# Optimization experiments

Hardware: AMD Instinct MI355X
Metric: run time of the kernel (lower is better)

## Reference

```python
import jax, jax.numpy as jnp
import numpy as np

B, L, H, D, VOC, C, P = 16, 256, 6, 768, 32000, 20, 1
d = D // H
MAXF = 20
BN_EPS = 1e-5


def setup_inputs() -> dict:
    key = jax.random.key(0)
    ks = jax.random.split(key, 8)
    doc_tids = jax.random.randint(ks[0], (B, L), 0, VOC)
    TFs = jax.random.uniform(ks[1], (B, L), dtype=jnp.float32) * 20.0 + 1.0
    DFs = jax.random.uniform(ks[2], (B, L), dtype=jnp.float32) * 1000.0 + 1.0
    emb = jax.random.normal(ks[3], (VOC, D), dtype=jnp.float32) * 0.02
    fcW = jax.random.normal(ks[4], (C + P, D), dtype=jnp.float32) * 0.02
    fcb = jnp.zeros((C + P,), dtype=jnp.float32)
    weiW = jax.random.normal(ks[5], (2, H), dtype=jnp.float32) * 0.1
    weib = jnp.zeros((2,), dtype=jnp.float32)
    return dict(doc_tids=doc_tids, TFs=TFs, DFs=DFs, emb=emb,
                fcW=fcW, fcb=fcb, weiW=weiW, weib=weib)


def _bn(x):
    # BatchNorm over channel axis 1 (H), batch stats over all other axes (train mode, affine=False)
    m = x.mean(axis=(0, 2, 3), keepdims=True)
    v = x.var(axis=(0, 2, 3), keepdims=True)
    return (x - m) * jax.lax.rsqrt(v + BN_EPS)


def _leaky9(x):
    return jnp.where(x >= 0, x, 9.0 * x)


def reference(doc_tids, TFs, DFs, emb, fcW, fcb, weiW, weib):
    # --- EmbbedingTFIDF (eval mode, dropout off): tf-idf weighted embedding lookup ---
    tf = jnp.minimum(TFs, float(MAXF))
    idf = jnp.log1p(1.0 / DFs)
    x = emb[doc_tids] * (tf * idf)[:, :, None]          # (B, L, D)
    valid = doc_tids != 0
    # model flips pad_mask with logical_not, then co_weights[pad_mask] = 0
    invalid = ~(valid[:, :, None] & valid[:, None, :])  # (B, L, L) True -> zero out
    mask = invalid[:, None, :, :]                       # broadcast over heads

    def split_heads(h):
        return h.reshape(B, L, H, d).transpose(0, 2, 1, 3)  # (B, H, L, d)

    Q = split_heads(x)
    K = Q
    V = Q

    # --- nearAttention (layers=1) ---
    Vn = _bn(V)
    # DistMatrix: pairwise Euclidean distance dist[b,h,i,j] = ||K_i - Q_j||
    Ksq = jnp.sum(K * K, axis=-1)[..., :, None]
    Qsq = jnp.sum(Q * Q, axis=-1)[..., None, :]
    cross = jnp.einsum('bhid,bhjd->bhij', K, Q)
    co = jnp.sqrt(jnp.maximum(Ksq + Qsq - 2.0 * cross, 1e-12))  # (B, H, L, L)
    # BatchNorm1d(H) over flattened (B, H, L*L) == per-H stats over (0,2,3)
    co = _leaky9(_bn(co))
    co = jnp.where(mask, 0.0, co)
    co = jax.nn.softmax(co, axis=-1)
    co = jnp.where(jnp.isnan(co), 0.0, co)
    V_out = jnp.einsum('bhij,bhjd->bhid', co, Vn)
    Q_out = _bn(jnp.einsum('bhij,bhjd->bhid', co, Q))
    K_out = _bn(jnp.einsum('bhij,bhjd->bhid', co, K))

    # --- head ---
    Vc = V_out.transpose(0, 2, 1, 3).reshape(B, L, D)       # catHiddens
    V_lgts = jax.nn.softmax(Vc @ fcW.T + fcb, axis=-1)      # (B, L, C+P)
    cw = jnp.swapaxes(co, -1, -2).reshape(B, L * L, H)      # transpose then contiguous reshape
    cw = jax.nn.softmax(cw @ weiW.T + weib, axis=-1)        # (B, L*L, 2)
    cw = cw.reshape(B, L, L, 2).sum(axis=-2, keepdims=True)[:, :, :, 0]  # (B, L, 1)
    cw = jax.nn.softmax(cw, axis=-1)                        # softmax over singleton -> ones (faithful)
    logits = (cw * V_lgts).sum(axis=1)[:, :C]               # (B, C)
    logits = jax.nn.softmax(logits, axis=-1)
    return logits
```

## Files before the change

### kernel.cpp

```cpp
#include <hip/hip_runtime.h>
#include <hip/hip_bf16.h>
#include <math.h>

#define OFF_XH   0UL
#define OFF_XT   1572864UL
#define OFF_VC   3145728UL
#define OFF_SQ   4718592UL
#define OFF_THS  4743168UL
#define OFF_PART 4767744UL
#define OFF_STAT 4780032UL
#define OFF_ACC  4780056UL
#define OFF_CTR  4780392UL
#define OFF_FCWB 4780396UL

typedef __attribute__((ext_vector_type(8))) __bf16 bf16x8;
typedef __attribute__((ext_vector_type(4))) float f32x4;
typedef __attribute__((ext_vector_type(8))) unsigned short u16x8;

__global__ __launch_bounds__(512) void k12_fused(const int* __restrict__ tids,
    const float* __restrict__ TF, const float* __restrict__ DF,
    const float* __restrict__ emb, unsigned short* __restrict__ xh,
    unsigned short* __restrict__ xT, float* __restrict__ sq,
    float* __restrict__ part, const float* __restrict__ fcW,
    unsigned short* __restrict__ fcWb, float* __restrict__ acc,
    unsigned int* __restrict__ ctr) {
  int jh = blockIdx.x, bh = blockIdx.y;
  int b = bh / 6, h = bh % 6;
  int tid = threadIdx.x;
  __shared__ unsigned short tile[32768];
  __shared__ float swd1[8], swd2[8], swv1[8], swv2[8];
  if (jh == 1) {
    if (tid < 168) {
      int idx = bh * 168 + tid;
      fcWb[idx] = __bfloat16_as_ushort(__float2bfloat16(fcW[idx]));
    }
  } else if (bh == 0) {
    if (tid < 336) acc[tid] = 0.0f;
    if (tid == 336) *ctr = 0u;
  }
  int sub = tid & 7, row0 = tid >> 3;
  int c16 = sub * 16;
  float ts1 = 0.0f, ts2 = 0.0f;
#pragma unroll
  for (int p = 0; p < 4; ++p) {
    int r = p * 64 + row0;
    int tok = b * 256 + r;
    int tv = tids[tok];
    float wgt = fminf(TF[tok], 20.0f) * log1pf(1.0f / DF[tok]);
    const float* er = emb + (size_t)tv * 768 + h * 128 + c16;
    float4 e0 = *(const float4*)er;
    float4 e1 = *(const float4*)(er + 4);
    float4 e2 = *(const float4*)(er + 8);
    float4 e3 = *(const float4*)(er + 12);
    float f[16] = {e0.x, e0.y, e0.z, e0.w, e1.x, e1.y, e1.z, e1.w,
                   e2.x, e2.y, e2.z, e2.w, e3.x, e3.y, e3.z, e3.w};
    u16x8 pk0, pk1;
    float s1 = 0.0f, s2 = 0.0f;
#pragma unroll
    for (int e = 0; e < 8; ++e) {
      __hip_bfloat16 hb = __float2bfloat16(f[e] * wgt);
      float g = __bfloat162float(hb);
      s1 += g; s2 += g * g;
      pk0[e] = __bfloat16_as_ushort(hb);
    }
#pragma unroll
    for (int e = 0; e < 8; ++e) {
      __hip_bfloat16 hb = __float2bfloat16(f[8 + e] * wgt);
      float g = __bfloat162float(hb);
      s1 += g; s2 += g * g;
      pk1[e] = __bfloat16_as_ushort(hb);
    }
    ts1 += s1; ts2 += s2;
    int rx = r & 7;
    *(u16x8*)&tile[r * 128 + (((sub * 2    ) ^ rx) * 8)] = pk0;
    *(u16x8*)&tile[r * 128 + (((sub * 2 + 1) ^ rx) * 8)] = pk1;
    if (jh == 0) {
      unsigned short* xo = xh + ((size_t)bh * 256 + r) * 128 + c16;
      *(u16x8*)xo = pk0;
      *(u16x8*)(xo + 8) = pk1;
    }
    s2 += __shfl_down(s2, 4); s2 += __shfl_down(s2, 2); s2 += __shfl_down(s2, 1);
    if (sub == 0)
      sq[(size_t)bh * 256 + r] = s2;
  }
  __syncthreads();
  if (jh == 1) {
    int ch = tid & 127, q = tid >> 7;
    int cc = ch >> 3, cs = ch & 7;
    unsigned int* xo = (unsigned int*)xT + ((size_t)bh * 128 + ch) * 128 + q * 32;
#pragma unroll
    for (int g = 0; g < 8; ++g) {
      unsigned int tmp[4];
#pragma unroll
      for (int k = 0; k < 4; ++k) {
        int t0 = q * 64 + (g * 4 + k) * 2;
        unsigned int lo = tile[ t0      * 128 + ((cc ^ ( t0      & 7)) * 8) + cs];
        unsigned int hi = tile[(t0 + 1) * 128 + ((cc ^ ((t0 + 1) & 7)) * 8) + cs];
        tmp[k] = lo | (hi << 16);
      }
      uint4 vv; vv.x = tmp[0]; vv.y = tmp[1]; vv.z = tmp[2]; vv.w = tmp[3];
      *(uint4*)(xo + g * 4) = vv;
    }
  }
  int w = tid >> 6, lane = tid & 63, quad = lane >> 4, l16 = lane & 15;
  const float* sqh = sq + (size_t)bh * 256;
  int it0 = w * 2;
  bf16x8 a2[2][4];
  float si2[2][4];
#pragma unroll
  for (int ith = 0; ith < 2; ++ith) {
    int ar = (it0 + ith) * 16 + l16, arx = ar & 7;
#pragma unroll
    for (int k0 = 0; k0 < 4; ++k0)
      a2[ith][k0] = *(const bf16x8*)&tile[ar * 128 + (((k0 * 4 + quad) ^ arx) * 8)];
#pragma unroll
    for (int r = 0; r < 4; ++r)
      si2[ith][r] = sqh[(it0 + ith) * 16 + quad * 4 + r];
  }
  float ls1 = 0.0f, ls2 = 0.0f;
#pragma unroll
  for (int jt = 0; jt < 8; ++jt) {
    int jr = jh * 128 + jt * 16 + l16, jrx = jr & 7;
    bf16x8 bfr[4];
#pragma unroll
    for (int k0 = 0; k0 < 4; ++k0)
      bfr[k0] = *(const bf16x8*)&tile[jr * 128 + (((k0 * 4 + quad) ^ jrx) * 8)];
    f32x4 acc0 = {0.0f, 0.0f, 0.0f, 0.0f}, acc1 = {0.0f, 0.0f, 0.0f, 0.0f};
#pragma unroll
    for (int k0 = 0; k0 < 4; ++k0) {
      acc0 = __builtin_amdgcn_mfma_f32_16x16x32_bf16(a2[0][k0], bfr[k0], acc0, 0, 0, 0);
      acc1 = __builtin_amdgcn_mfma_f32_16x16x32_bf16(a2[1][k0], bfr[k0], acc1, 0, 0, 0);
    }
    float sj = sqh[jr];
#pragma unroll
    for (int r = 0; r < 4; ++r) {
      float cv0 = sqrtf(fmaxf(si2[0][r] + sj - 2.0f * acc0[r], 1e-12f));
      float cv1 = sqrtf(fmaxf(si2[1][r] + sj - 2.0f * acc1[r], 1e-12f));
      ls1 += cv0 + cv1;
      ls2 += cv0 * cv0 + cv1 * cv1;
    }
  }
#pragma unroll
  for (int off = 32; off >= 1; off >>= 1) {
    ls1 += __shfl_down(ls1, off);
    ls2 += __shfl_down(ls2, off);
    ts1 += __shfl_down(ts1, off);
    ts2 += __shfl_down(ts2, off);
  }
  if (lane == 0) { swd1[w] = ls1; swd2[w] = ls2; swv1[w] = ts1; swv2[w] = ts2; }
  __syncthreads();
  if (tid == 0) {
    float d1 = 0.0f, d2 = 0.0f, v1 = 0.0f, v2 = 0.0f;
#pragma unroll
    for (int i = 0; i < 8; ++i) { d1 += swd1[i]; d2 += swd2[i]; v1 += swv1[i]; v2 += swv2[i]; }
    part[192 + (bh * 2 + jh) * 2 + 0] = d1;
    part[192 + (bh * 2 + jh) * 2 + 1] = d2;
    if (jh == 0) { part[bh * 2] = v1; part[bh * 2 + 1] = v2; }
  }
}

__global__ __launch_bounds__(256, 4) void k45_fused(const unsigned short* __restrict__ xh,
    const unsigned short* __restrict__ xT, const int* __restrict__ tids,
    const float* __restrict__ sq, const float* __restrict__ part,
    unsigned short* __restrict__ vc16) {
  int bid = blockIdx.x;
  int xcd = bid & 7, idx = bid >> 3;
  int bh = xcd * 12 + idx % 12;
  int p = idx / 12;
  int b = bh / 6, h = bh % 6;
  int tid = threadIdx.x, w = tid >> 6, lane = tid & 63;
  int quad = lane >> 4, l16 = lane & 15;
  int I = p * 16;
  __shared__ float svld[256];
  __shared__ float ssq[256];
  __shared__ unsigned short cot[16][264];
  __shared__ float smax[16][4];
  __shared__ float ssum[16][4];
  __shared__ float sstat[4];
  svld[tid] = (tids[b * 256 + tid] != 0) ? 1.0f : 0.0f;
  ssq[tid] = sq[(size_t)bh * 256 + tid];
  if (w == 0) {
    float c1 = 0.0f, c2 = 0.0f;
    if (lane < 32) {
      int bb = lane >> 1, jj = lane & 1;
      c1 = part[192 + ((bb * 6 + h) * 2 + jj) * 2 + 0];
      c2 = part[192 + ((bb * 6 + h) * 2 + jj) * 2 + 1];
    }
#pragma unroll
    for (int off = 16; off >= 1; off >>= 1) {
      c1 += __shfl_down(c1, off);
      c2 += __shfl_down(c2, off);
    }
    float v1 = 0.0f, v2 = 0.0f;
    if (lane < 16) {
      v1 = part[(lane * 6 + h) * 2 + 0];
      v2 = part[(lane * 6 + h) * 2 + 1];
    }
#pragma unroll
    for (int off = 8; off >= 1; off >>= 1) {
      v1 += __shfl_down(v1, off);
      v2 += __shfl_down(v2, off);
    }
    if (lane == 0) {
      float mean = c1 / 1048576.0f;
      float var = c2 / 1048576.0f - mean * mean;
      sstat[0] = mean;
      sstat[1] = rsqrtf(var + 1e-5f);
      float mv = v1 / 524288.0f;
      float vv = v2 / 524288.0f - mv * mv;
      sstat[2] = mv;
      sstat[3] = rsqrtf(vv + 1e-5f);
    }
  }
  const __bf16* xb = (const __bf16*)xh + (size_t)bh * 256 * 128;
  bf16x8 a[4];
#pragma unroll
  for (int k0 = 0; k0 < 4; ++k0)
    a[k0] = *(const bf16x8*)(xb + (size_t)(I + l16) * 128 + k0 * 32 + quad * 8);
  __syncthreads();
  float m = sstat[0], rsc = sstat[1];
  float rv[4], si[4];
#pragma unroll
  for (int r = 0; r < 4; ++r) {
    rv[r] = svld[I + quad * 4 + r];
    si[r] = ssq[I + quad * 4 + r];
  }
  float y[4][4];
#pragma unroll
  for (int tl = 0; tl < 4; ++tl) {
    int t = w * 4 + tl;
    f32x4 acc = {0.0f, 0.0f, 0.0f, 0.0f};
#pragma unroll
    for (int k0 = 0; k0 < 4; ++k0) {
      bf16x8 bfr = *(const bf16x8*)(xb + (size_t)(t * 16 + l16) * 128 + k0 * 32 + quad * 8);
      acc = __builtin_amdgcn_mfma_f32_16x16x32_bf16(a[k0], bfr, acc, 0, 0, 0);
    }
    float sj = ssq[t * 16 + l16];
    float cvld = svld[t * 16 + l16];
#pragma unroll
    for (int r = 0; r < 4; ++r) {
      float cv = sqrtf(fmaxf(si[r] + sj - 2.0f * acc[r], 1e-12f));
      float yv = (cv - m) * rsc;
      yv = yv >= 0.0f ? yv : 9.0f * yv;
      y[tl][r] = yv * rv[r] * cvld;
    }
  }
#pragma unroll
  for (int r = 0; r < 4; ++r) {
    float mx = fmaxf(fmaxf(y[0][r], y[1][r]), fmaxf(y[2][r], y[3][r]));
#pragma unroll
    for (int off = 1; off <= 8; off <<= 1) mx = fmaxf(mx, __shfl_xor(mx, off));
    if (l16 == 0) smax[quad * 4 + r][w] = mx;
  }
  __syncthreads();
  float gmx[4];
#pragma unroll
  for (int r = 0; r < 4; ++r) {
    int row = quad * 4 + r;
    gmx[r] = fmaxf(fmaxf(smax[row][0], smax[row][1]), fmaxf(smax[row][2], smax[row][3]));
    float s = 0.0f;
#pragma unroll
    for (int tl = 0; tl < 4; ++tl) { y[tl][r] = expf(y[tl][r] - gmx[r]); s += y[tl][r]; }
#pragma unroll
    for (int off = 1; off <= 8; off <<= 1) s += __shfl_xor(s, off);
    if (l16 == 0) ssum[row][w] = s;
  }
  __syncthreads();
#pragma unroll
  for (int r = 0; r < 4; ++r) {
    int row = quad * 4 + r;
    float gs = ssum[row][0] + ssum[row][1] + ssum[row][2] + ssum[row][3];
    float inv = 1.0f / gs;
#pragma unroll
    for (int tl = 0; tl < 4; ++tl)
      cot[row][w * 64 + tl * 16 + l16] =
          __bfloat16_as_ushort(__float2bfloat16(y[tl][r] * inv));
  }
  __syncthreads();
  bf16x8 a2[8];
#pragma unroll
  for (int k0 = 0; k0 < 8; ++k0)
    a2[k0] = *(const bf16x8*)&cot[l16][k0 * 32 + quad * 8];
  const __bf16* xbT = (const __bf16*)xT + (size_t)bh * 128 * 256;
  float mv = sstat[2], rvs = sstat[3];
  float rm = rvs * mv;
  size_t vbase = ((size_t)(b * 256 + I + quad * 4)) * 768 + h * 128;
#pragma unroll
  for (int jl = 0; jl < 2; ++jl) {
    int ch = (w * 2 + jl) * 16 + l16;
    const __bf16* brow = xbT + (size_t)ch * 256;
    f32x4 vacc = {0.0f, 0.0f, 0.0f, 0.0f};
#pragma unroll
    for (int k0 = 0; k0 < 8; ++k0) {
      bf16x8 bfr = *(const bf16x8*)(brow + k0 * 32 + quad * 8);
      vacc = __builtin_amdgcn_mfma_f32_16x16x32_bf16(a2[k0], bfr, vacc, 0, 0, 0);
    }
#pragma unroll
    for (int r = 0; r < 4; ++r) {
      float ov = rvs * vacc[r] - rm;
      vc16[vbase + (size_t)r * 768 + ch] = __bfloat16_as_ushort(__float2bfloat16(ov));
    }
  }
}

__global__ __launch_bounds__(256) void k5b6_lgts(const unsigned short* __restrict__ vc16,
    const unsigned short* __restrict__ fcWb, const float* __restrict__ fcb,
    float* __restrict__ acc, unsigned int* __restrict__ ctr, float* __restrict__ out) {
  int b = blockIdx.x >> 2, qa = blockIdx.x & 3;
  int tid = threadIdx.x, w = tid >> 6, lane = tid & 63;
  int quad = lane >> 4, l16 = lane & 15;
  int tok0 = b * 256 + qa * 64 + w * 16;
  int c1c = (l16 < 5) ? (16 + l16) : 20;
  const __bf16* vb = (const __bf16*)vc16;
  const __bf16* w0 = (const __bf16*)fcWb + (size_t)l16 * 768;
  const __bf16* w1 = (const __bf16*)fcWb + (size_t)c1c * 768;
  f32x4 ac0 = {0.0f, 0.0f, 0.0f, 0.0f}, ac1 = {0.0f, 0.0f, 0.0f, 0.0f};
#pragma unroll
  for (int k0 = 0; k0 < 24; ++k0) {
    int ko = k0 * 32 + quad * 8;
    bf16x8 af = *(const bf16x8*)(vb + (size_t)(tok0 + l16) * 768 + ko);
    bf16x8 b0 = *(const bf16x8*)(w0 + ko);
    bf16x8 b1 = *(const bf16x8*)(w1 + ko);
    ac0 = __builtin_amdgcn_mfma_f32_16x16x32_bf16(af, b0, ac0, 0, 0, 0);
    ac1 = __builtin_amdgcn_mfma_f32_16x16x32_bf16(af, b1, ac1, 0, 0, 0);
  }
  float bias0 = fcb[l16];
  float bias1 = (l16 < 5) ? fcb[16 + l16] : 0.0f;
  float p0s = 0.0f, p1s = 0.0f;
#pragma unroll
  for (int r = 0; r < 4; ++r) {
    float lg0 = ac0[r] + bias0;
    float lg1 = (l16 < 5) ? (ac1[r] + bias1) : -1e30f;
    float mx = fmaxf(lg0, lg1);
#pragma unroll
    for (int off = 1; off <= 8; off <<= 1) mx = fmaxf(mx, __shfl_xor(mx, off));
    float e0 = expf(lg0 - mx), e1 = expf(lg1 - mx);
    float s = e0 + e1;
#pragma unroll
    for (int off = 1; off <= 8; off <<= 1) s += __shfl_xor(s, off);
    float inv = 1.0f / s;
    p0s += e0 * inv;
    p1s += e1 * inv;
  }
  p0s += __shfl_xor(p0s, 16); p0s += __shfl_xor(p0s, 32);
  p1s += __shfl_xor(p1s, 16); p1s += __shfl_xor(p1s, 32);
  __shared__ float sacc[4][21];
  __shared__ unsigned int sdone;
  if (quad == 0) sacc[w][l16] = p0s;
  if (quad == 1 && l16 < 5) sacc[w][16 + l16] = p1s;
  __syncthreads();
  if (tid < 21) {
    float s = sacc[0][tid] + sacc[1][tid] + sacc[2][tid] + sacc[3][tid];
    atomicAdd(&acc[b * 21 + tid], s);
  }
  __syncthreads();
  if (tid == 0) {
    __threadfence();
    sdone = atomicAdd(ctr, 1u);
  }
  __syncthreads();
  if (sdone == 63u && tid < 16) {
    float v[20];
    float mx = -1e30f;
#pragma unroll
    for (int c = 0; c < 20; ++c) {
      v[c] = atomicAdd(&acc[tid * 21 + c], 0.0f);
      mx = fmaxf(mx, v[c]);
    }
    float s = 0.0f;
#pragma unroll
    for (int c = 0; c < 20; ++c) { v[c] = expf(v[c] - mx); s += v[c]; }
    float inv = 1.0f / s;
#pragma unroll
    for (int c = 0; c < 20; ++c) out[tid * 20 + c] = v[c] * inv;
  }
}

extern "C" void kernel_launch(void* const* d_in, const int* in_sizes, int n_in,
                              void* d_out, int out_size, void* d_ws, size_t ws_size,
                              hipStream_t stream) {
  const int*   tids = (const int*)d_in[0];
  const float* TF   = (const float*)d_in[1];
  const float* DF   = (const float*)d_in[2];
  const float* emb  = (const float*)d_in[3];
  const float* fcW  = (const float*)d_in[4];
  const float* fcb  = (const float*)d_in[5];
  float* out = (float*)d_out;
  float* ws  = (float*)d_ws;
  unsigned short* xh   = (unsigned short*)(ws + OFF_XH);
  unsigned short* xT   = (unsigned short*)(ws + OFF_XT);
  unsigned short* vc   = (unsigned short*)(ws + OFF_VC);
  unsigned short* fcWb = (unsigned short*)(ws + OFF_FCWB);
  float* sq    = ws + OFF_SQ;
  float* part  = ws + OFF_PART;
  float* acc   = ws + OFF_ACC;
  unsigned int* ctr = (unsigned int*)(ws + OFF_CTR);

  k12_fused<<<dim3(2, 96), 512, 0, stream>>>(tids, TF, DF, emb, xh, xT, sq, part,
                                             fcW, fcWb, acc, ctr);
  k45_fused<<<1536, 256, 0, stream>>>(xh, xT, tids, sq, part, vc);
  k5b6_lgts<<<64, 256, 0, stream>>>(vc, fcWb, fcb, acc, ctr, out);
}
```

Baseline: 193.6 us.

## Fuse attention and logits kernels into one per-row-tile kernel over all heads

The attention kernel and the classifier-logits kernel are merged. Each 512-thread block now handles one batch and a 16-row tile across all six heads sequentially, keeping the concatenated V output in shared memory instead of writing it to global memory. The fc projection, per-token softmax and batch accumulation then run from shared memory. This removes a kernel launch and the global round trip of the V buffer. In exchange the grid shrinks from 1536 to 256 blocks, and the loop over heads is serialised with extra barriers, which may reduce parallelism and latency hiding.

```diff
diff --git a/kernel.cpp b/kernel.cpp
--- a/kernel.cpp
+++ b/kernel.cpp
@@ -4,11 +4,8 @@
 
 #define OFF_XH   0UL
 #define OFF_XT   1572864UL
-#define OFF_VC   3145728UL
 #define OFF_SQ   4718592UL
-#define OFF_THS  4743168UL
 #define OFF_PART 4767744UL
-#define OFF_STAT 4780032UL
 #define OFF_ACC  4780056UL
 #define OFF_CTR  4780392UL
 #define OFF_FCWB 4780396UL
@@ -159,27 +156,34 @@
   }
 }
 
-__global__ __launch_bounds__(256, 4) void k45_fused(const unsigned short* __restrict__ xh,
+__global__ __launch_bounds__(512) void k456_fused(const unsigned short* __restrict__ xh,
     const unsigned short* __restrict__ xT, const int* __restrict__ tids,
     const float* __restrict__ sq, const float* __restrict__ part,
-    unsigned short* __restrict__ vc16) {
+    const unsigned short* __restrict__ fcWb, const float* __restrict__ fcb,
+    float* __restrict__ acc, unsigned int* __restrict__ ctr, float* __restrict__ out) {
   int bid = blockIdx.x;
   int xcd = bid & 7, idx = bid >> 3;
-  int bh = xcd * 12 + idx % 12;
-  int p = idx / 12;
-  int b = bh / 6, h = bh % 6;
+  int b = xcd * 2 + (idx >> 4);
+  int p = idx & 15;
   int tid = threadIdx.x, w = tid >> 6, lane = tid & 63;
   int quad = lane >> 4, l16 = lane & 15;
   int I = p * 16;
   __shared__ float svld[256];
-  __shared__ float ssq[256];
+  __shared__ float ssqall[1536];
   __shared__ unsigned short cot[16][264];
-  __shared__ float smax[16][4];
-  __shared__ float ssum[16][4];
-  __shared__ float sstat[4];
-  svld[tid] = (tids[b * 256 + tid] != 0) ? 1.0f : 0.0f;
-  ssq[tid] = sq[(size_t)bh * 256 + tid];
-  if (w == 0) {
+  __shared__ float smax[16][8];
+  __shared__ float ssum[16][8];
+  __shared__ float sstat[24];
+  __shared__ unsigned short vct[16][776];
+  __shared__ float sacc[16][22];
+  __shared__ float facc[21];
+  __shared__ unsigned int sdone;
+  if (tid < 256) svld[tid] = (tids[b * 256 + tid] != 0) ? 1.0f : 0.0f;
+  for (int i = tid; i < 1536; i += 512) ssqall[i] = sq[(size_t)b * 1536 + i];
+  if (tid < 352) ((float*)sacc)[tid] = 0.0f;
+  if (tid >= 352 && tid < 373) facc[tid - 352] = 0.0f;
+  if (w < 6) {
+    int h = w;
     float c1 = 0.0f, c2 = 0.0f;
     if (lane < 32) {
       int bb = lane >> 1, jj = lane & 1;
@@ -204,90 +208,92 @@
     if (lane == 0) {
       float mean = c1 / 1048576.0f;
       float var = c2 / 1048576.0f - mean * mean;
-      sstat[0] = mean;
-      sstat[1] = rsqrtf(var + 1e-5f);
+      sstat[h * 4 + 0] = mean;
+      sstat[h * 4 + 1] = rsqrtf(var + 1e-5f);
       float mv = v1 / 524288.0f;
       float vv = v2 / 524288.0f - mv * mv;
-      sstat[2] = mv;
-      sstat[3] = rsqrtf(vv + 1e-5f);
-    }
-  }
-  const __bf16* xb = (const __bf16*)xh + (size_t)bh * 256 * 128;
-  bf16x8 a[4];
-#pragma unroll
-  for (int k0 = 0; k0 < 4; ++k0)
-    a[k0] = *(const bf16x8*)(xb + (size_t)(I + l16) * 128 + k0 * 32 + quad * 8);
-  __syncthreads();
-  float m = sstat[0], rsc = sstat[1];
-  float rv[4], si[4];
-#pragma unroll
-  for (int r = 0; r < 4; ++r) {
-    rv[r] = svld[I + quad * 4 + r];
-    si[r] = ssq[I + quad * 4 + r];
-  }
-  float y[4][4];
-#pragma unroll
-  for (int tl = 0; tl < 4; ++tl) {
-    int t = w * 4 + tl;
-    f32x4 acc = {0.0f, 0.0f, 0.0f, 0.0f};
-#pragma unroll
-    for (int k0 = 0; k0 < 4; ++k0) {
-      bf16x8 bfr = *(const bf16x8*)(xb + (size_t)(t * 16 + l16) * 128 + k0 * 32 + quad * 8);
-      acc = __builtin_amdgcn_mfma_f32_16x16x32_bf16(a[k0], bfr, acc, 0, 0, 0);
-    }
-    float sj = ssq[t * 16 + l16];
-    float cvld = svld[t * 16 + l16];
-#pragma unroll
-    for (int r = 0; r < 4; ++r) {
-      float cv = sqrtf(fmaxf(si[r] + sj - 2.0f * acc[r], 1e-12f));
-      float yv = (cv - m) * rsc;
-      yv = yv >= 0.0f ? yv : 9.0f * yv;
-      y[tl][r] = yv * rv[r] * cvld;
-    }
-  }
-#pragma unroll
-  for (int r = 0; r < 4; ++r) {
-    float mx = fmaxf(fmaxf(y[0][r], y[1][r]), fmaxf(y[2][r], y[3][r]));
-#pragma unroll
-    for (int off = 1; off <= 8; off <<= 1) mx = fmaxf(mx, __shfl_xor(mx, off));
-    if (l16 == 0) smax[quad * 4 + r][w] = mx;
-  }
-  __syncthreads();
-  float gmx[4];
-#pragma unroll
-  for (int r = 0; r < 4; ++r) {
-    int row = quad * 4 + r;
-    gmx[r] = fmaxf(fmaxf(smax[row][0], smax[row][1]), fmaxf(smax[row][2], smax[row][3]));
-    float s = 0.0f;
-#pragma unroll
-    for (int tl = 0; tl < 4; ++tl) { y[tl][r] = expf(y[tl][r] - gmx[r]); s += y[tl][r]; }
-#pragma unroll
-    for (int off = 1; off <= 8; off <<= 1) s += __shfl_xor(s, off);
-    if (l16 == 0) ssum[row][w] = s;
-  }
-  __syncthreads();
-#pragma unroll
-  for (int r = 0; r < 4; ++r) {
-    int row = quad * 4 + r;
-    float gs = ssum[row][0] + ssum[row][1] + ssum[row][2] + ssum[row][3];
-    float inv = 1.0f / gs;
-#pragma unroll
-    for (int tl = 0; tl < 4; ++tl)
-      cot[row][w * 64 + tl * 16 + l16] =
-          __bfloat16_as_ushort(__float2bfloat16(y[tl][r] * inv));
-  }
-  __syncthreads();
-  bf16x8 a2[8];
-#pragma unroll
-  for (int k0 = 0; k0 < 8; ++k0)
-    a2[k0] = *(const bf16x8*)&cot[l16][k0 * 32 + quad * 8];
-  const __bf16* xbT = (const __bf16*)xT + (size_t)bh * 128 * 256;
-  float mv = sstat[2], rvs = sstat[3];
-  float rm = rvs * mv;
-  size_t vbase = ((size_t)(b * 256 + I + quad * 4)) * 768 + h * 128;
-#pragma unroll
-  for (int jl = 0; jl < 2; ++jl) {
-    int ch = (w * 2 + jl) * 16 + l16;
+      sstat[h * 4 + 2] = mv;
+      sstat[h * 4 + 3] = rsqrtf(vv + 1e-5f);
+    }
+  }
+  __syncthreads();
+  for (int h = 0; h < 6; ++h) {
+    int bh = b * 6 + h;
+    const __bf16* xb = (const __bf16*)xh + (size_t)bh * 256 * 128;
+    bf16x8 a[4];
+#pragma unroll
+    for (int k0 = 0; k0 < 4; ++k0)
+      a[k0] = *(const bf16x8*)(xb + (size_t)(I + l16) * 128 + k0 * 32 + quad * 8);
+    float m = sstat[h * 4 + 0], rsc = sstat[h * 4 + 1];
+    float rv[4], si[4];
+#pragma unroll
+    for (int r = 0; r < 4; ++r) {
+      rv[r] = svld[I + quad * 4 + r];
+      si[r] = ssqall[h * 256 + I + quad * 4 + r];
+    }
+    float y[2][4];
+#pragma unroll
+    for (int tl = 0; tl < 2; ++tl) {
+      int t = w * 2 + tl;
+      f32x4 accd = {0.0f, 0.0f, 0.0f, 0.0f};
+#pragma unroll
+      for (int k0 = 0; k0 < 4; ++k0) {
+        bf16x8 bfr = *(const bf16x8*)(xb + (size_t)(t * 16 + l16) * 128 + k0 * 32 + quad * 8);
+        accd = __builtin_amdgcn_mfma_f32_16x16x32_bf16(a[k0], bfr, accd, 0, 0, 0);
+      }
+      float sj = ssqall[h * 256 + t * 16 + l16];
+      float cvld = svld[t * 16 + l16];
+#pragma unroll
+      for (int r = 0; r < 4; ++r) {
+        float cv = sqrtf(fmaxf(si[r] + sj - 2.0f * accd[r], 1e-12f));
+        float yv = (cv - m) * rsc;
+        yv = yv >= 0.0f ? yv : 9.0f * yv;
+        y[tl][r] = yv * rv[r] * cvld;
+      }
+    }
+#pragma unroll
+    for (int r = 0; r < 4; ++r) {
+      float mx = fmaxf(y[0][r], y[1][r]);
+#pragma unroll
+      for (int off = 1; off <= 8; off <<= 1) mx = fmaxf(mx, __shfl_xor(mx, off));
+      if (l16 == 0) smax[quad * 4 + r][w] = mx;
+    }
+    __syncthreads();
+    float gmx[4];
+#pragma unroll
+    for (int r = 0; r < 4; ++r) {
+      int row = quad * 4 + r;
+      float g0 = fmaxf(fmaxf(smax[row][0], smax[row][1]), fmaxf(smax[row][2], smax[row][3]));
+      float g1 = fmaxf(fmaxf(smax[row][4], smax[row][5]), fmaxf(smax[row][6], smax[row][7]));
+      gmx[r] = fmaxf(g0, g1);
+      float s = 0.0f;
+#pragma unroll
+      for (int tl = 0; tl < 2; ++tl) { y[tl][r] = expf(y[tl][r] - gmx[r]); s += y[tl][r]; }
+#pragma unroll
+      for (int off = 1; off <= 8; off <<= 1) s += __shfl_xor(s, off);
+      if (l16 == 0) ssum[row][w] = s;
+    }
+    __syncthreads();
+#pragma unroll
+    for (int r = 0; r < 4; ++r) {
+      int row = quad * 4 + r;
+      float gs = (ssum[row][0] + ssum[row][1] + ssum[row][2] + ssum[row][3])
+               + (ssum[row][4] + ssum[row][5] + ssum[row][6] + ssum[row][7]);
+      float inv = 1.0f / gs;
+#pragma unroll
+      for (int tl = 0; tl < 2; ++tl)
+        cot[row][w * 32 + tl * 16 + l16] =
+            __bfloat16_as_ushort(__float2bfloat16(y[tl][r] * inv));
+    }
+    __syncthreads();
+    bf16x8 a2[8];
+#pragma unroll
+    for (int k0 = 0; k0 < 8; ++k0)
+      a2[k0] = *(const bf16x8*)&cot[l16][k0 * 32 + quad * 8];
+    const __bf16* xbT = (const __bf16*)xT + (size_t)bh * 128 * 256;
+    float mv = sstat[h * 4 + 2], rvs = sstat[h * 4 + 3];
+    float rm = rvs * mv;
+    int ch = w * 16 + l16;
     const __bf16* brow = xbT + (size_t)ch * 256;
     f32x4 vacc = {0.0f, 0.0f, 0.0f, 0.0f};
 #pragma unroll
@@ -298,68 +304,50 @@
 #pragma unroll
     for (int r = 0; r < 4; ++r) {
       float ov = rvs * vacc[r] - rm;
-      vc16[vbase + (size_t)r * 768 + ch] = __bfloat16_as_ushort(__float2bfloat16(ov));
-    }
-  }
-}
-
-__global__ __launch_bounds__(256) void k5b6_lgts(const unsigned short* __restrict__ vc16,
-    const unsigned short* __restrict__ fcWb, const float* __restrict__ fcb,
-    float* __restrict__ acc, unsigned int* __restrict__ ctr, float* __restrict__ out) {
-  int b = blockIdx.x >> 2, qa = blockIdx.x & 3;
-  int tid = threadIdx.x, w = tid >> 6, lane = tid & 63;
-  int quad = lane >> 4, l16 = lane & 15;
-  int tok0 = b * 256 + qa * 64 + w * 16;
+      vct[quad * 4 + r][h * 128 + ch] = __bfloat16_as_ushort(__float2bfloat16(ov));
+    }
+    __syncthreads();
+  }
   int c1c = (l16 < 5) ? (16 + l16) : 20;
-  const __bf16* vb = (const __bf16*)vc16;
   const __bf16* w0 = (const __bf16*)fcWb + (size_t)l16 * 768;
   const __bf16* w1 = (const __bf16*)fcWb + (size_t)c1c * 768;
   f32x4 ac0 = {0.0f, 0.0f, 0.0f, 0.0f}, ac1 = {0.0f, 0.0f, 0.0f, 0.0f};
 #pragma unroll
-  for (int k0 = 0; k0 < 24; ++k0) {
-    int ko = k0 * 32 + quad * 8;
-    bf16x8 af = *(const bf16x8*)(vb + (size_t)(tok0 + l16) * 768 + ko);
+  for (int s = 0; s < 3; ++s) {
+    int ko = (w * 3 + s) * 32 + quad * 8;
+    bf16x8 af = *(const bf16x8*)&vct[l16][ko];
     bf16x8 b0 = *(const bf16x8*)(w0 + ko);
     bf16x8 b1 = *(const bf16x8*)(w1 + ko);
     ac0 = __builtin_amdgcn_mfma_f32_16x16x32_bf16(af, b0, ac0, 0, 0, 0);
     ac1 = __builtin_amdgcn_mfma_f32_16x16x32_bf16(af, b1, ac1, 0, 0, 0);
   }
-  float bias0 = fcb[l16];
-  float bias1 = (l16 < 5) ? fcb[16 + l16] : 0.0f;
-  float p0s = 0.0f, p1s = 0.0f;
 #pragma unroll
   for (int r = 0; r < 4; ++r) {
-    float lg0 = ac0[r] + bias0;
-    float lg1 = (l16 < 5) ? (ac1[r] + bias1) : -1e30f;
-    float mx = fmaxf(lg0, lg1);
-#pragma unroll
-    for (int off = 1; off <= 8; off <<= 1) mx = fmaxf(mx, __shfl_xor(mx, off));
-    float e0 = expf(lg0 - mx), e1 = expf(lg1 - mx);
-    float s = e0 + e1;
-#pragma unroll
-    for (int off = 1; off <= 8; off <<= 1) s += __shfl_xor(s, off);
+    atomicAdd(&sacc[quad * 4 + r][l16], ac0[r]);
+    if (l16 < 5) atomicAdd(&sacc[quad * 4 + r][16 + l16], ac1[r]);
+  }
+  __syncthreads();
+  if (tid < 16) {
+    int row = tid;
+    float lg[21], mx = -1e30f;
+#pragma unroll
+    for (int c = 0; c < 21; ++c) { lg[c] = sacc[row][c] + fcb[c]; mx = fmaxf(mx, lg[c]); }
+    float s = 0.0f;
+#pragma unroll
+    for (int c = 0; c < 21; ++c) { lg[c] = expf(lg[c] - mx); s += lg[c]; }
     float inv = 1.0f / s;
-    p0s += e0 * inv;
-    p1s += e1 * inv;
-  }
-  p0s += __shfl_xor(p0s, 16); p0s += __shfl_xor(p0s, 32);
-  p1s += __shfl_xor(p1s, 16); p1s += __shfl_xor(p1s, 32);
-  __shared__ float sacc[4][21];
-  __shared__ unsigned int sdone;
-  if (quad == 0) sacc[w][l16] = p0s;
-  if (quad == 1 && l16 < 5) sacc[w][16 + l16] = p1s;
-  __syncthreads();
-  if (tid < 21) {
-    float s = sacc[0][tid] + sacc[1][tid] + sacc[2][tid] + sacc[3][tid];
-    atomicAdd(&acc[b * 21 + tid], s);
-  }
+#pragma unroll
+    for (int c = 0; c < 21; ++c) atomicAdd(&facc[c], lg[c] * inv);
+  }
+  __syncthreads();
+  if (tid < 21) atomicAdd(&acc[b * 21 + tid], facc[tid]);
   __syncthreads();
   if (tid == 0) {
     __threadfence();
     sdone = atomicAdd(ctr, 1u);
   }
   __syncthreads();
-  if (sdone == 63u && tid < 16) {
+  if (sdone == 255u && tid < 16) {
     float v[20];
     float mx = -1e30f;
 #pragma unroll
@@ -389,7 +377,6 @@
   float* ws  = (float*)d_ws;
   unsigned short* xh   = (unsigned short*)(ws + OFF_XH);
   unsigned short* xT   = (unsigned short*)(ws + OFF_XT);
-  unsigned short* vc   = (unsigned short*)(ws + OFF_VC);
   unsigned short* fcWb = (unsigned short*)(ws + OFF_FCWB);
   float* sq    = ws + OFF_SQ;
   float* part  = ws + OFF_PART;
@@ -398,6 +385,5 @@
 
   k12_fused<<<dim3(2, 96), 512, 0, stream>>>(tids, TF, DF, emb, xh, xT, sq, part,
                                              fcW, fcWb, acc, ctr);
-  k45_fused<<<1536, 256, 0, stream>>>(xh, xT, tids, sq, part, vc);
-  k5b6_lgts<<<64, 256, 0, stream>>>(vc, fcWb, fcb, acc, ctr, out);
+  k456_fused<<<256, 512, 0, stream>>>(xh, xT, tids, sq, part, fcWb, fcb, acc, ctr, out);
 }
```

After: 222.0 us. 14.7% more time.
